# Optimization experiments

Measured on AMD Instinct MI355X. Metric: run time of the kernel, lower is better.

The kernel has to match this reference:

```python
import jax, jax.numpy as jnp
import numpy as np

N = 20000
E = N * 16
K = 6  # DynamicEdgeConv default k


def feast_conv(x, edge_index, W, u, c, b):
    # PyG FeaStConv with aggr='mean' and added self-loops.
    # q_h = softmax_h(u_h . (x_j - x_i) + c_h); msg = sum_h q_h * (W_h x_j)
    n = x.shape[0]
    heads = u.shape[1]
    out_ch = W.shape[1] // heads
    loops = jnp.arange(n)
    src = jnp.concatenate([edge_index[0], loops])  # x_j (source)
    dst = jnp.concatenate([edge_index[1], loops])  # x_i (target)
    xi = x[dst]
    xj = x[src]
    q = jax.nn.softmax((xj - xi) @ u + c, axis=-1)           # [E+N, H]
    m = (xj @ W).reshape(-1, heads, out_ch)                   # [E+N, H, O]
    msg = (m * q[..., None]).sum(axis=1)                      # [E+N, O]
    agg = jax.ops.segment_sum(msg, dst, num_segments=n)
    cnt = jax.ops.segment_sum(jnp.ones((dst.shape[0],), x.dtype), dst, num_segments=n)
    return agg / jnp.maximum(cnt, 1.0)[:, None] + b


def dynamic_edge_conv(x, W1, b1, W2, b2, k=K):
    # knn_graph (Euclidean, no self-loops) + EdgeConv with max aggregation.
    n = x.shape[0]
    sq = jnp.sum(x * x, axis=1)
    d = sq[:, None] + sq[None, :] - 2.0 * (x @ x.T)           # [N, N] squared dists
    d = d.at[jnp.arange(n), jnp.arange(n)].set(jnp.inf)       # loop=False
    idx = jax.lax.stop_gradient(jax.lax.top_k(-d, k)[1])      # [N, k] neighbors of i
    xj = x[idx]                                               # [N, k, C]
    xi = x[:, None, :]
    tmp = jnp.concatenate([jnp.broadcast_to(xi, xj.shape), xj - xi], axis=-1)
    h = jax.nn.relu(tmp @ W1 + b1) @ W2 + b2                  # mlp on each edge
    return h.max(axis=1)                                      # scatter-max == max over fixed k


def forward(x, edge_index, params):
    (cW1, cu1, cc1, cb1, cW3, cu3, cc3, cb3,
     e1W1, e1b1, e1W2, e1b2, e2W1, e2b1, e2W2, e2b2,
     l1W, l1b, l2W, l2b, l3W, l3b, oW, ob) = params
    x1 = jax.nn.relu(feast_conv(x, edge_index, cW1, cu1, cc1, cb1))      # [N,16]
    y1 = jax.nn.relu(dynamic_edge_conv(x1, e1W1, e1b1, e1W2, e1b2))      # [N,32]
    cat0 = jnp.concatenate([x1, y1], axis=1)                              # [N,48]
    # conv2 output is dead code in the original forward (overwritten), skipped
    y2 = jax.nn.relu(dynamic_edge_conv(y1, e2W1, e2b1, e2W2, e2b2))      # [N,32]
    x3 = jax.nn.relu(feast_conv(cat0, edge_index, cW3, cu3, cc3, cb3))   # [N,64]
    cat1 = jnp.concatenate([x3, y2], axis=1)                              # [N,96]
    h = jax.nn.relu(cat1 @ l1W + l1b)
    h = jax.nn.relu(h @ l2W + l2b)
    h = jax.nn.relu(h @ l3W + l3b)  # double relu in source is idempotent
    return jax.nn.sigmoid(h @ oW + ob)                                    # [N,1]


def setup_inputs() -> dict:
    key = jax.random.key(0)
    ks = jax.random.split(key, 20)
    rn = lambda k, s: jax.random.normal(k, s, jnp.float32) * 0.1
    z = lambda s: jnp.zeros(s, jnp.float32)
    return {
        "x": jax.random.normal(ks[0], (N, 16), jnp.float32),
        "edge_index": jax.random.randint(ks[1], (2, E), 0, N, dtype=jnp.int32),
        # conv1: FeaStConv(16 -> 16, heads=1)
        "cW1": rn(ks[2], (16, 16)), "cu1": rn(ks[3], (16, 1)), "cc1": z((1,)), "cb1": z((16,)),
        # conv3: FeaStConv(48 -> 64, heads=1)
        "cW3": rn(ks[4], (48, 64)), "cu3": rn(ks[5], (48, 1)), "cc3": z((1,)), "cb3": z((64,)),
        # edge1 mlp: Linear(2*16, 32), Linear(32, 32)
        "e1W1": rn(ks[6], (32, 32)), "e1b1": z((32,)), "e1W2": rn(ks[7], (32, 32)), "e1b2": z((32,)),
        # edge2 mlp: Linear(2*32, 32), Linear(32, 32)
        "e2W1": rn(ks[8], (64, 32)), "e2b1": z((32,)), "e2W2": rn(ks[9], (32, 32)), "e2b2": z((32,)),
        # dense head
        "l1W": rn(ks[10], (96, 96)), "l1b": z((96,)),
        "l2W": rn(ks[11], (96, 32)), "l2b": z((32,)),
        "l3W": rn(ks[12], (32, 8)), "l3b": z((8,)),
        "oW": rn(ks[13], (8, 1)), "ob": z((1,)),
    }


def reference(x, edge_index, cW1, cu1, cc1, cb1, cW3, cu3, cc3, cb3,
              e1W1, e1b1, e1W2, e1b2, e2W1, e2b1, e2W2, e2b2,
              l1W, l1b, l2W, l2b, l3W, l3b, oW, ob):
    params = (cW1, cu1, cc1, cb1, cW3, cu3, cc3, cb3,
              e1W1, e1b1, e1W2, e1b2, e2W1, e2b1, e2W2, e2b2,
              l1W, l1b, l2W, l2b, l3W, l3b, oW, ob)
    return forward(x, edge_index, params)
```

## Files before the change

kernel.cpp:

```cpp
#include <hip/hip_runtime.h>
#include <cstdint>

constexpr int Nn = 20000;
constexpr int Ee = 320000;
constexpr int KN = 6;

__global__ __launch_bounds__(256) void scatter16(const float* __restrict__ x,
                                                 const int* __restrict__ ei,
                                                 float* __restrict__ agg,
                                                 int* __restrict__ cnt) {
  int tid = blockIdx.x * 256 + threadIdx.x;
  int e = tid >> 4, c = tid & 15;
  if (e >= Ee) return;
  int s = ei[e], d = ei[Ee + e];
  unsafeAtomicAdd(&agg[d * 16 + c], x[s * 16 + c]);
  if (c == 0) atomicAdd(&cnt[d], 1);
}

__global__ __launch_bounds__(256) void feast1_fin(const float* __restrict__ x,
                                                  const float* __restrict__ agg,
                                                  const int* __restrict__ cnt,
                                                  const float* __restrict__ W,
                                                  const float* __restrict__ b,
                                                  float* __restrict__ x1,
                                                  float* __restrict__ sq) {
  __shared__ float sW[256];
  __shared__ float sb[16];
  sW[threadIdx.x] = W[threadIdx.x];
  if (threadIdx.x < 16) sb[threadIdx.x] = b[threadIdx.x];
  __syncthreads();
  int n = blockIdx.x * 256 + threadIdx.x;
  if (n >= Nn) return;
  float inv = 1.0f / (float)(cnt[n] + 1);
  float v[16];
#pragma unroll
  for (int c = 0; c < 16; ++c) v[c] = (agg[n * 16 + c] + x[n * 16 + c]) * inv;
  float s = 0.0f;
#pragma unroll
  for (int o = 0; o < 16; ++o) {
    float a = sb[o];
#pragma unroll
    for (int c = 0; c < 16; ++c) a = fmaf(v[c], sW[c * 16 + o], a);
    a = fmaxf(a, 0.0f);
    x1[n * 16 + o] = a;
    s = fmaf(a, a, s);
  }
  sq[n] = s;
}

__device__ __forceinline__ void insert6(float d, int j, float (&bd)[KN], int (&bi)[KN]) {
  bd[KN - 1] = d;
  bi[KN - 1] = j;
#pragma unroll
  for (int k = KN - 1; k >= 1; --k) {
    if (bd[k] < bd[k - 1]) {
      float td = bd[k]; bd[k] = bd[k - 1]; bd[k - 1] = td;
      int ti = bi[k]; bi[k] = bi[k - 1]; bi[k - 1] = ti;
    }
  }
}

template <int C, int U, int TPB>
__global__ __launch_bounds__(TPB) void knn_part(const float* __restrict__ xf,
                                                const float* __restrict__ sq,
                                                float* __restrict__ pd,
                                                int* __restrict__ pi, int chunk) {
  const int row = blockIdx.x * TPB + (int)threadIdx.x;
  const int p = blockIdx.y;
  const int j0 = p * chunk;
  int j1 = j0 + chunk;
  if (j1 > Nn) j1 = Nn;

  float xi[C];
  {
    const float* src = xf + (size_t)(row < Nn ? row : 0) * C;
#pragma unroll
    for (int c = 0; c < C; ++c) xi[c] = src[c];
  }
  float bd[KN];
  int bi[KN];
#pragma unroll
  for (int k = 0; k < KN; ++k) { bd[k] = __builtin_inff(); bi[k] = -1; }

  int j = j0;
  for (; j + U <= j1; j += U) {
    float sv[U];
#pragma unroll
    for (int u = 0; u < U; ++u) {
      const float* xjp = xf + (size_t)(j + u) * C;
      float sqj = sq[j + u];
      float acc = 0.0f;
#pragma unroll
      for (int c = 0; c < C; ++c) acc = fmaf(xi[c], xjp[c], acc);
      float d = fmaf(-2.0f, acc, sqj);
      sv[u] = (j + u == row) ? __builtin_inff() : d;
    }
#pragma unroll
    for (int u = 0; u < U; ++u) {
      if (sv[u] < bd[KN - 1]) insert6(sv[u], j + u, bd, bi);
    }
  }
  for (; j < j1; ++j) {
    const float* xjp = xf + (size_t)j * C;
    float sqj = sq[j];
    float acc = 0.0f;
#pragma unroll
    for (int c = 0; c < C; ++c) acc = fmaf(xi[c], xjp[c], acc);
    float d = fmaf(-2.0f, acc, sqj);
    d = (j == row) ? __builtin_inff() : d;
    if (d < bd[KN - 1]) insert6(d, j, bd, bi);
  }

  if (row < Nn) {
    size_t base = ((size_t)p * Nn + row) * KN;
    for (int k = 0; k < KN; ++k) { pd[base + k] = bd[k]; pi[base + k] = bi[k]; }
  }
}

__global__ __launch_bounds__(256) void knn_merge(const float* __restrict__ pd,
                                                 const int* __restrict__ pi,
                                                 int* __restrict__ idx, int P) {
  int row = blockIdx.x * 256 + threadIdx.x;
  if (row >= Nn) return;
  float bd[KN];
  int bi[KN];
#pragma unroll
  for (int k = 0; k < KN; ++k) { bd[k] = __builtin_inff(); bi[k] = -1; }
  for (int p = 0; p < P; ++p) {
    size_t base = ((size_t)p * Nn + row) * KN;
#pragma unroll
    for (int k = 0; k < KN; ++k) {
      float d = pd[base + k];
      int id = pi[base + k];
      if (d < bd[KN - 1]) {
        bd[KN - 1] = d; bi[KN - 1] = id;
#pragma unroll
        for (int m = KN - 1; m >= 1; --m) {
          if (bd[m] < bd[m - 1]) {
            float td = bd[m]; bd[m] = bd[m - 1]; bd[m - 1] = td;
            int ti = bi[m]; bi[m] = bi[m - 1]; bi[m - 1] = ti;
          }
        }
      }
    }
  }
  for (int k = 0; k < KN; ++k) idx[row * KN + k] = bi[k];
}

__global__ __launch_bounds__(256) void edge_mlp1(const float* __restrict__ xin,
                                                 const int* __restrict__ idx,
                                                 const float* __restrict__ W1,
                                                 const float* __restrict__ b1,
                                                 const float* __restrict__ W2,
                                                 const float* __restrict__ b2,
                                                 float* __restrict__ yout,
                                                 float* __restrict__ sqout) {
  __shared__ float sW1[1024], sW2[1024], sb1[32], sb2[32];
  __shared__ float xv[8][16], tmp[8][32], hv[8][32];
  int t = threadIdx.x & 31, g = threadIdx.x >> 5;
  for (int i = threadIdx.x; i < 1024; i += 256) { sW1[i] = W1[i]; sW2[i] = W2[i]; }
  if (threadIdx.x < 32) { sb1[threadIdx.x] = b1[threadIdx.x]; sb2[threadIdx.x] = b2[threadIdx.x]; }
  int node = blockIdx.x * 8 + g;
  bool valid = node < Nn;
  int nn = valid ? node : 0;
  if (t < 16) { float v = xin[nn * 16 + t]; xv[g][t] = v; tmp[g][t] = v; }
  __syncthreads();
  float acc = -__builtin_inff();
  for (int k = 0; k < KN; ++k) {
    int j = idx[nn * KN + k];
    if (t < 16) tmp[g][16 + t] = xin[j * 16 + t] - xv[g][t];
    __syncthreads();
    float h = sb1[t];
#pragma unroll
    for (int c = 0; c < 32; ++c) h = fmaf(tmp[g][c], sW1[c * 32 + t], h);
    h = fmaxf(h, 0.0f);
    hv[g][t] = h;
    __syncthreads();
    float o = sb2[t];
#pragma unroll
    for (int c = 0; c < 32; ++c) o = fmaf(hv[g][c], sW2[c * 32 + t], o);
    acc = fmaxf(acc, o);
  }
  float yv = fmaxf(acc, 0.0f);
  if (valid) yout[node * 32 + t] = yv;
  float s = yv * yv;
  s += __shfl_xor(s, 16, 32);
  s += __shfl_xor(s, 8, 32);
  s += __shfl_xor(s, 4, 32);
  s += __shfl_xor(s, 2, 32);
  s += __shfl_xor(s, 1, 32);
  if (valid && t == 0) sqout[node] = s;
}

__global__ __launch_bounds__(256) void edge_mlp2(const float* __restrict__ yin,
                                                 const int* __restrict__ idx,
                                                 const float* __restrict__ W1,
                                                 const float* __restrict__ b1,
                                                 const float* __restrict__ W2,
                                                 const float* __restrict__ b2,
                                                 float* __restrict__ yout) {
  __shared__ float sW1[2048], sW2[1024], sb1[32], sb2[32];
  __shared__ float xv[8][32], tmp[8][64], hv[8][32];
  int t = threadIdx.x & 31, g = threadIdx.x >> 5;
  for (int i = threadIdx.x; i < 2048; i += 256) sW1[i] = W1[i];
  for (int i = threadIdx.x; i < 1024; i += 256) sW2[i] = W2[i];
  if (threadIdx.x < 32) { sb1[threadIdx.x] = b1[threadIdx.x]; sb2[threadIdx.x] = b2[threadIdx.x]; }
  int node = blockIdx.x * 8 + g;
  bool valid = node < Nn;
  int nn = valid ? node : 0;
  { float v = yin[nn * 32 + t]; xv[g][t] = v; tmp[g][t] = v; }
  __syncthreads();
  float acc = -__builtin_inff();
  for (int k = 0; k < KN; ++k) {
    int j = idx[nn * KN + k];
    tmp[g][32 + t] = yin[j * 32 + t] - xv[g][t];
    __syncthreads();
    float h = sb1[t];
#pragma unroll
    for (int c = 0; c < 64; ++c) h = fmaf(tmp[g][c], sW1[c * 32 + t], h);
    h = fmaxf(h, 0.0f);
    hv[g][t] = h;
    __syncthreads();
    float o = sb2[t];
#pragma unroll
    for (int c = 0; c < 32; ++c) o = fmaf(hv[g][c], sW2[c * 32 + t], o);
    acc = fmaxf(acc, o);
  }
  if (valid) yout[node * 32 + t] = fmaxf(acc, 0.0f);
}

__global__ __launch_bounds__(256) void scatter48(const float* __restrict__ x1,
                                                 const float* __restrict__ y1,
                                                 const int* __restrict__ ei,
                                                 float* __restrict__ agg) {
  int tid = blockIdx.x * 256 + threadIdx.x;
  int e = tid / 48, c = tid - e * 48;
  if (e >= Ee) return;
  int s = ei[e], d = ei[Ee + e];
  float v = (c < 16) ? x1[s * 16 + c] : y1[s * 32 + (c - 16)];
  unsafeAtomicAdd(&agg[d * 48 + c], v);
}

__global__ __launch_bounds__(256) void feast3_fin(const float* __restrict__ x1,
                                                  const float* __restrict__ y1,
                                                  const float* __restrict__ agg,
                                                  const int* __restrict__ cnt,
                                                  const float* __restrict__ W,
                                                  const float* __restrict__ b,
                                                  float* __restrict__ x3) {
  __shared__ float sW[3072];
  __shared__ float sb[64];
  for (int i = threadIdx.x; i < 3072; i += 256) sW[i] = W[i];
  if (threadIdx.x < 64) sb[threadIdx.x] = b[threadIdx.x];
  __syncthreads();
  int n = blockIdx.x * 256 + threadIdx.x;
  if (n >= Nn) return;
  float inv = 1.0f / (float)(cnt[n] + 1);
  float v[48];
#pragma unroll
  for (int c = 0; c < 16; ++c) v[c] = (agg[n * 48 + c] + x1[n * 16 + c]) * inv;
#pragma unroll
  for (int c = 16; c < 48; ++c) v[c] = (agg[n * 48 + c] + y1[n * 32 + (c - 16)]) * inv;
  for (int o = 0; o < 64; ++o) {
    float a = sb[o];
#pragma unroll
    for (int c = 0; c < 48; ++c) a = fmaf(v[c], sW[c * 64 + o], a);
    x3[n * 64 + o] = fmaxf(a, 0.0f);
  }
}

__global__ __launch_bounds__(256) void final_mlp(const float* __restrict__ x3,
                                                 const float* __restrict__ y2,
                                                 const float* __restrict__ l1W,
                                                 const float* __restrict__ l1b,
                                                 const float* __restrict__ l2W,
                                                 const float* __restrict__ l2b,
                                                 const float* __restrict__ l3W,
                                                 const float* __restrict__ l3b,
                                                 const float* __restrict__ oW,
                                                 const float* __restrict__ ob,
                                                 float* __restrict__ out) {
  __shared__ float cat[2][96], h1[2][96], h2[2][32], h3[2][8];
  int g = threadIdx.x >> 7, t = threadIdx.x & 127;
  int node = blockIdx.x * 2 + g;
  bool valid = node < Nn;
  int nn = valid ? node : 0;
  if (t < 96) cat[g][t] = (t < 64) ? x3[nn * 64 + t] : y2[nn * 32 + (t - 64)];
  __syncthreads();
  if (t < 96) {
    float a = l1b[t];
#pragma unroll
    for (int c = 0; c < 96; ++c) a = fmaf(cat[g][c], l1W[c * 96 + t], a);
    h1[g][t] = fmaxf(a, 0.0f);
  }
  __syncthreads();
  if (t < 32) {
    float a = l2b[t];
#pragma unroll
    for (int c = 0; c < 96; ++c) a = fmaf(h1[g][c], l2W[c * 32 + t], a);
    h2[g][t] = fmaxf(a, 0.0f);
  }
  __syncthreads();
  if (t < 8) {
    float a = l3b[t];
#pragma unroll
    for (int c = 0; c < 32; ++c) a = fmaf(h2[g][c], l3W[c * 8 + t], a);
    h3[g][t] = fmaxf(a, 0.0f);
  }
  __syncthreads();
  if (t == 0 && valid) {
    float a = ob[0];
#pragma unroll
    for (int c = 0; c < 8; ++c) a = fmaf(h3[g][c], oW[c], a);
    out[node] = 1.0f / (1.0f + expf(-a));
  }
}

extern "C" void kernel_launch(void* const* d_in, const int* in_sizes, int n_in,
                              void* d_out, int out_size, void* d_ws, size_t ws_size,
                              hipStream_t stream) {
  const float* x = (const float*)d_in[0];
  const int* ei = (const int*)d_in[1];
  const float* cW1 = (const float*)d_in[2];
  const float* cb1 = (const float*)d_in[5];
  const float* cW3 = (const float*)d_in[6];
  const float* cb3 = (const float*)d_in[9];
  const float* e1W1 = (const float*)d_in[10];
  const float* e1b1 = (const float*)d_in[11];
  const float* e1W2 = (const float*)d_in[12];
  const float* e1b2 = (const float*)d_in[13];
  const float* e2W1 = (const float*)d_in[14];
  const float* e2b1 = (const float*)d_in[15];
  const float* e2W2 = (const float*)d_in[16];
  const float* e2b2 = (const float*)d_in[17];
  const float* l1W = (const float*)d_in[18];
  const float* l1b = (const float*)d_in[19];
  const float* l2W = (const float*)d_in[20];
  const float* l2b = (const float*)d_in[21];
  const float* l3W = (const float*)d_in[22];
  const float* l3b = (const float*)d_in[23];
  const float* oW = (const float*)d_in[24];
  const float* ob = (const float*)d_in[25];
  float* out = (float*)d_out;

  char* p = (char*)d_ws;
  auto alloc = [&](size_t bytes) {
    char* r = p;
    p += (bytes + 255) & ~(size_t)255;
    return r;
  };
  float* x1 = (float*)alloc((size_t)Nn * 16 * 4);
  float* y1 = (float*)alloc((size_t)Nn * 32 * 4);
  float* y2 = (float*)alloc((size_t)Nn * 32 * 4);
  float* x3 = (float*)alloc((size_t)Nn * 64 * 4);
  float* agg = (float*)alloc((size_t)Nn * 48 * 4);
  int* cnt = (int*)alloc((size_t)Nn * 4);
  float* sqb = (float*)alloc((size_t)Nn * 4);
  int* idx1 = (int*)alloc((size_t)Nn * KN * 4);
  int* idx2 = (int*)alloc((size_t)Nn * KN * 4);
  size_t fixed_bytes = (size_t)(p - (char*)d_ws);
  size_t per_chunk = (size_t)Nn * KN * 4 * 2 + 512;
  int P1 = 16;
  int P2 = 12;
  if (fixed_bytes + (size_t)P1 * per_chunk > ws_size) {
    size_t avail = ws_size > fixed_bytes ? ws_size - fixed_bytes : 0;
    int pmax = (int)(avail / per_chunk);
    P1 = pmax < 1 ? 1 : pmax;
    if (P1 > 16) P1 = 16;
    if (P2 > P1) P2 = P1;
  }
  float* pd = (float*)alloc((size_t)P1 * Nn * KN * 4);
  int* pi = (int*)alloc((size_t)P1 * Nn * KN * 4);
  int chunk1 = (Nn + P1 - 1) / P1;
  int chunk2 = (Nn + P2 - 1) / P2;

  hipMemsetAsync(agg, 0, (size_t)Nn * 16 * 4, stream);
  hipMemsetAsync(cnt, 0, (size_t)Nn * 4, stream);
  scatter16<<<(Ee * 16) / 256, 256, 0, stream>>>(x, ei, agg, cnt);
  feast1_fin<<<(Nn + 255) / 256, 256, 0, stream>>>(x, agg, cnt, cW1, cb1, x1, sqb);

  {
    dim3 grid((Nn + 255) / 256, P1);
    knn_part<16, 4, 256><<<grid, 256, 0, stream>>>(x1, sqb, pd, pi, chunk1);
    knn_merge<<<(Nn + 255) / 256, 256, 0, stream>>>(pd, pi, idx1, P1);
  }

  edge_mlp1<<<(Nn + 7) / 8, 256, 0, stream>>>(x1, idx1, e1W1, e1b1, e1W2, e1b2, y1, sqb);

  {
    dim3 grid((Nn + 255) / 256, P2);
    knn_part<32, 2, 256><<<grid, 256, 0, stream>>>(y1, sqb, pd, pi, chunk2);
    knn_merge<<<(Nn + 255) / 256, 256, 0, stream>>>(pd, pi, idx2, P2);
  }

  edge_mlp2<<<(Nn + 7) / 8, 256, 0, stream>>>(y1, idx2, e2W1, e2b1, e2W2, e2b2, y2);

  hipMemsetAsync(agg, 0, (size_t)Nn * 48 * 4, stream);
  scatter48<<<(Ee * 48) / 256, 256, 0, stream>>>(x1, y1, ei, agg);
  feast3_fin<<<(Nn + 255) / 256, 256, 0, stream>>>(x1, y1, agg, cnt, cW3, cb3, x3);

  final_mlp<<<(Nn + 1) / 2, 256, 0, stream>>>(x3, y2, l1W, l1b, l2W, l2b, l3W, l3b,
                                              oW, ob, out);
}
```

Measured before the change: 1.480 ms.

## Batch kNN distances per 32-candidate segment with bitmask-driven warp-uniform insertion

```diff
diff --git a/kernel.cpp b/kernel.cpp
--- a/kernel.cpp
+++ b/kernel.cpp
@@ -60,12 +60,15 @@
   }
 }
 
-template <int C, int U, int TPB>
+template <int C, int TPB>
 __global__ __launch_bounds__(TPB) void knn_part(const float* __restrict__ xf,
                                                 const float* __restrict__ sq,
                                                 float* __restrict__ pd,
                                                 int* __restrict__ pi, int chunk) {
-  const int row = blockIdx.x * TPB + (int)threadIdx.x;
+  constexpr int SEG = 32;
+  __shared__ float sd[SEG * TPB];
+  const int tid = (int)threadIdx.x;
+  const int row = blockIdx.x * TPB + tid;
   const int p = blockIdx.y;
   const int j0 = p * chunk;
   int j1 = j0 + chunk;
@@ -82,33 +85,30 @@
 #pragma unroll
   for (int k = 0; k < KN; ++k) { bd[k] = __builtin_inff(); bi[k] = -1; }
 
-  int j = j0;
-  for (; j + U <= j1; j += U) {
-    float sv[U];
-#pragma unroll
-    for (int u = 0; u < U; ++u) {
-      const float* xjp = xf + (size_t)(j + u) * C;
-      float sqj = sq[j + u];
+  for (int jseg = j0; jseg < j1; jseg += SEG) {
+    unsigned m = 0;
+    const float worst = bd[KN - 1];
+#pragma unroll
+    for (int t = 0; t < SEG; ++t) {
+      const int j = jseg + t;
+      const float* xjp = xf + (size_t)j * C;
+      const float sqj = sq[j];
       float acc = 0.0f;
 #pragma unroll
       for (int c = 0; c < C; ++c) acc = fmaf(xi[c], xjp[c], acc);
       float d = fmaf(-2.0f, acc, sqj);
-      sv[u] = (j + u == row) ? __builtin_inff() : d;
+      d = (j == row) ? __builtin_inff() : d;
+      sd[t * TPB + tid] = d;
+      m |= (d < worst) ? (1u << t) : 0u;
     }
-#pragma unroll
-    for (int u = 0; u < U; ++u) {
-      if (sv[u] < bd[KN - 1]) insert6(sv[u], j + u, bd, bi);
+    while (__any(m != 0)) {
+      if (m != 0) {
+        const int t = __builtin_ctz(m);
+        m &= m - 1;
+        const float d = sd[t * TPB + tid];
+        if (d < bd[KN - 1]) insert6(d, jseg + t, bd, bi);
+      }
     }
-  }
-  for (; j < j1; ++j) {
-    const float* xjp = xf + (size_t)j * C;
-    float sqj = sq[j];
-    float acc = 0.0f;
-#pragma unroll
-    for (int c = 0; c < C; ++c) acc = fmaf(xi[c], xjp[c], acc);
-    float d = fmaf(-2.0f, acc, sqj);
-    d = (j == row) ? __builtin_inff() : d;
-    if (d < bd[KN - 1]) insert6(d, j, bd, bi);
   }
 
   if (row < Nn) {
@@ -360,19 +360,16 @@
   int* idx2 = (int*)alloc((size_t)Nn * KN * 4);
   size_t fixed_bytes = (size_t)(p - (char*)d_ws);
   size_t per_chunk = (size_t)Nn * KN * 4 * 2 + 512;
-  int P1 = 16;
-  int P2 = 12;
-  if (fixed_bytes + (size_t)P1 * per_chunk > ws_size) {
+  int P = 16;
+  if (fixed_bytes + (size_t)P * per_chunk > ws_size) {
     size_t avail = ws_size > fixed_bytes ? ws_size - fixed_bytes : 0;
     int pmax = (int)(avail / per_chunk);
-    P1 = pmax < 1 ? 1 : pmax;
-    if (P1 > 16) P1 = 16;
-    if (P2 > P1) P2 = P1;
-  }
-  float* pd = (float*)alloc((size_t)P1 * Nn * KN * 4);
-  int* pi = (int*)alloc((size_t)P1 * Nn * KN * 4);
-  int chunk1 = (Nn + P1 - 1) / P1;
-  int chunk2 = (Nn + P2 - 1) / P2;
+    P = pmax < 1 ? 1 : pmax;
+    if (P > 16) P = 16;
+  }
+  float* pd = (float*)alloc((size_t)P * Nn * KN * 4);
+  int* pi = (int*)alloc((size_t)P * Nn * KN * 4);
+  int chunk = (((Nn + P - 1) / P) + 31) & ~31;
 
   hipMemsetAsync(agg, 0, (size_t)Nn * 16 * 4, stream);
   hipMemsetAsync(cnt, 0, (size_t)Nn * 4, stream);
@@ -380,17 +377,17 @@
   feast1_fin<<<(Nn + 255) / 256, 256, 0, stream>>>(x, agg, cnt, cW1, cb1, x1, sqb);
 
   {
-    dim3 grid((Nn + 255) / 256, P1);
-    knn_part<16, 4, 256><<<grid, 256, 0, stream>>>(x1, sqb, pd, pi, chunk1);
-    knn_merge<<<(Nn + 255) / 256, 256, 0, stream>>>(pd, pi, idx1, P1);
+    dim3 grid((Nn + 255) / 256, P);
+    knn_part<16, 256><<<grid, 256, 0, stream>>>(x1, sqb, pd, pi, chunk);
+    knn_merge<<<(Nn + 255) / 256, 256, 0, stream>>>(pd, pi, idx1, P);
   }
 
   edge_mlp1<<<(Nn + 7) / 8, 256, 0, stream>>>(x1, idx1, e1W1, e1b1, e1W2, e1b2, y1, sqb);
 
   {
-    dim3 grid((Nn + 255) / 256, P2);
-    knn_part<32, 2, 256><<<grid, 256, 0, stream>>>(y1, sqb, pd, pi, chunk2);
-    knn_merge<<<(Nn + 255) / 256, 256, 0, stream>>>(pd, pi, idx2, P2);
+    dim3 grid((Nn + 255) / 256, P);
+    knn_part<32, 256><<<grid, 256, 0, stream>>>(y1, sqb, pd, pi, chunk);
+    knn_merge<<<(Nn + 255) / 256, 256, 0, stream>>>(pd, pi, idx2, P);
   }
 
   edge_mlp2<<<(Nn + 7) / 8, 256, 0, stream>>>(y1, idx2, e2W1, e2b1, e2W2, e2b2, y2);
```

After: 2.498 ms. 1.69x slower.
